# Kernel optimization log

Hardware: AMD Instinct MI355X
Metric: run time of the kernel (lower is better)

## Reference

```python
import math
import jax, jax.numpy as jnp
from jax import lax
import numpy as np

NUM_HEADS = 8

def conv2d(x, w, b):
    # x: [N,C,H,W], w: [O,I,3,3], padding=1 == SAME
    y = lax.conv_general_dilated(x, w, (1, 1), 'SAME',
                                 dimension_numbers=('NCHW', 'OIHW', 'NCHW'))
    return y + b[None, :, None, None]

def setup_inputs() -> dict:
    key = jax.random.key(0)
    ks = jax.random.split(key, 10)
    B, L, C = 64, 196, 768
    K, R = 8192, 8
    return {
        'in_feas': jax.random.normal(ks[0], (B, L, C), jnp.float32),
        'cur_f': 4,
        'codebook': jax.random.normal(ks[1], (K, C), jnp.float32),
        'att_w': jax.random.normal(ks[2], (R, C, 3, 3), jnp.float32) * 0.02,
        'att_b': jnp.zeros((R,), jnp.float32),
        'ex_w': jax.random.normal(ks[3], (1, C, 3, 3), jnp.float32) * 0.02,
        'ex_b': jnp.zeros((1,), jnp.float32),
        'qkv_w': jax.random.normal(ks[4], (3 * C, C), jnp.float32) * 0.02,
        'qkv_b': jnp.zeros((3 * C,), jnp.float32),
        'proj_w': jax.random.normal(ks[5], (C, C), jnp.float32) * 0.02,
        'proj_b': jnp.zeros((C,), jnp.float32),
    }

def attention(x, qkv_w, qkv_b, proj_w, proj_b):
    # x: [B, N, C], standard multi-head self-attention
    B, N, C = x.shape
    dh = C // NUM_HEADS
    qkv = x @ qkv_w.T + qkv_b                          # [B,N,3C]
    qkv = qkv.reshape(B, N, 3, NUM_HEADS, dh).transpose(2, 0, 3, 1, 4)
    q, k, v = qkv[0], qkv[1], qkv[2]                   # [B,H,N,dh]
    attn = jax.nn.softmax(jnp.einsum('bhnd,bhmd->bhnm', q, k) * (dh ** -0.5), axis=-1)
    out = jnp.einsum('bhnm,bhmd->bhnd', attn, v)
    out = out.transpose(0, 2, 1, 3).reshape(B, N, C)
    return out @ proj_w.T + proj_b

def reference(in_feas, cur_f, codebook, att_w, att_b, ex_w, ex_b,
              qkv_w, qkv_b, proj_w, proj_b):
    B, L, C = in_feas.shape
    h = int(math.sqrt(L)); w = L // h
    R = att_w.shape[0]

    # ---- Vector quantization: cdist + argmin + codebook gather ----
    flat = in_feas.reshape(-1, C)                      # [B*L, C]
    d = (jnp.sum(flat * flat, axis=1, keepdims=True)
         - 2.0 * flat @ codebook.T
         + jnp.sum(codebook * codebook, axis=1)[None, :])   # [B*L, K]
    idx = jnp.argmin(d, axis=1)                        # [B*L]
    quant = codebook[idx]                              # gather
    vq = flat + lax.stop_gradient(quant - flat)        # straight-through
    enc = idx.reshape(-1, h, w)                        # [B, h, w]

    # ---- Motion excitation (cur_f > 1) ----
    Bp = B // cur_f
    x = in_feas.reshape(Bp, cur_f, L, C)
    diff = x - jnp.concatenate([x[:, :1], x[:, :-1]], axis=1)  # frame diff, first frame zero
    dmap = diff.reshape(-1, L, C).transpose(0, 2, 1).reshape(-1, C, h, w)
    mm = conv2d(dmap, ex_w, ex_b).reshape(Bp, cur_f, L)
    mm = jax.nn.softmax(mm, axis=-1)
    motion = (x * mm[..., None]).reshape(-1, C)
    vq = vq + motion

    # ---- Aggregation: region attention conv + masked pooling (as one einsum) ----
    xm = vq.reshape(B, L, C).transpose(0, 2, 1).reshape(B, C, h, w)
    region_mask = conv2d(xm, att_w, att_b)             # [B,R,h,w]
    regions = jnp.einsum('bchw,brhw->bcr', xm, region_mask) / (h * w)  # [B,C,R]
    vd = regions.transpose(0, 2, 1)                    # [B,R,C]

    # ---- Interaction: self-attention over T*S region tokens ----
    seq = vd.reshape(Bp, cur_f * R, C)
    seq = attention(seq, qkv_w, qkv_b, proj_w, proj_b)
    vd = seq.reshape(-1, R, C)                         # [B,R,C]
    return (vd, enc, region_mask)
```

## Files before the change

kernel.cpp:

```cpp
#include <hip/hip_runtime.h>
#include <math.h>

#define B_   64
#define L_   196
#define C_   768
#define K_   8192
#define R_   8
#define HW_  14
#define M_   (B_*L_)
#define NH_  8
#define DH_  96
#define BP_  16
#define NT_  32

typedef unsigned short ushort_t;
typedef __attribute__((ext_vector_type(8))) short short8v;
typedef __attribute__((ext_vector_type(4))) float f32x4;
typedef __attribute__((ext_vector_type(4))) int   i32x4;

#define BIGF __uint_as_float(0x7F000000u)

__device__ inline float wave_reduce_sum(float v) {
    #pragma unroll
    for (int o = 32; o >= 1; o >>= 1) v += __shfl_xor(v, o, 64);
    return v;
}
__device__ inline float wave_reduce_max(float v) {
    #pragma unroll
    for (int o = 32; o >= 1; o >>= 1) v = fmaxf(v, __shfl_xor(v, o, 64));
    return v;
}

__device__ inline ushort_t f2bf_rne(float f) {
    unsigned u = __float_as_uint(f);
    unsigned r = u + 0x7fffu + ((u >> 16) & 1u);
    return (ushort_t)(r >> 16);
}
__device__ inline float bf2f(ushort_t h) { return __uint_as_float(((unsigned)h) << 16); }

__device__ inline char q8(float f, float s) {
    int q = __float2int_rn(f * s);
    return (char)(q < -127 ? -127 : (q > 127 ? 127 : q));
}

__device__ inline void gload_lds16(const void* gsrc, void* ldst) {
    __builtin_amdgcn_global_load_lds(
        (const __attribute__((address_space(1))) unsigned int*)gsrc,
        (__attribute__((address_space(3))) unsigned int*)ldst, 16, 0, 0);
}

__global__ __launch_bounds__(256) void cbq_kernel(const float* __restrict__ CB,
                                                  char* __restrict__ CBq,
                                                  float* __restrict__ cnq) {
    __shared__ float xs[16 * 776];
    const int t = threadIdx.x;
    const int blk = blockIdx.x;
    const float4* src = (const float4*)(CB + (size_t)blk * 16 * C_);
    #pragma unroll
    for (int i = 0; i < 12; ++i) {
        int idx4 = t + i * 256;
        int r = idx4 / 192, c4 = idx4 - r * 192;
        ((float4*)(xs + r * 776))[c4] = src[idx4];
    }
    __syncthreads();
    #pragma unroll
    for (int i = 0; i < 3; ++i) {
        int s = t + i * 256;
        int kb = s >> 6, l = s & 63;
        int row = l & 15;
        int k0 = kb * 64 + ((l >> 4) << 4);
        union { char c[16]; i32x4 v; } Q;
        #pragma unroll
        for (int e = 0; e < 16; ++e) Q.c[e] = q8(xs[row * 776 + k0 + e], 32.f);
        *(i32x4*)&CBq[(((size_t)blk * 12 + kb) << 10) + l * 16] = Q.v;
    }
    int row = t & 15, chunk = t >> 4;
    float sum = 0.f;
    #pragma unroll
    for (int j = 0; j < 48; ++j) { float v = xs[row * 776 + chunk * 48 + j]; sum += v * v; }
    sum += __shfl_xor(sum, 16, 64);
    sum += __shfl_xor(sum, 32, 64);
    __shared__ float red[4][16];
    if ((t & 63) < 16) red[t >> 6][t & 15] = sum;
    __syncthreads();
    if (t < 16) cnq[blk * 16 + t] = (red[0][t] + red[1][t] + red[2][t] + red[3][t]) * 1024.f;
}

__global__ __launch_bounds__(256) void aq_kernel(const float* __restrict__ X,
                                                 char* __restrict__ Aq) {
    __shared__ float xs[16 * 776];
    const int t = threadIdx.x;
    const int rg = blockIdx.x;
    const float4* src = (const float4*)(X + (size_t)rg * 16 * C_);
    #pragma unroll
    for (int i = 0; i < 12; ++i) {
        int idx4 = t + i * 256;
        int r = idx4 / 192, c4 = idx4 - r * 192;
        ((float4*)(xs + r * 776))[c4] = src[idx4];
    }
    __syncthreads();
    #pragma unroll
    for (int i = 0; i < 3; ++i) {
        int s = t + i * 256;
        int kb = s >> 6, l = s & 63;
        int row = l & 15;
        int k0 = kb * 64 + ((l >> 4) << 4);
        union { char c[16]; i32x4 v; } Q;
        #pragma unroll
        for (int e = 0; e < 16; ++e) Q.c[e] = q8(xs[row * 776 + k0 + e], 32.f);
        *(i32x4*)&Aq[(((size_t)rg * 12 + kb) << 10) + l * 16] = Q.v;
    }
}

__global__ __launch_bounds__(256) void wsplit_kernel(const float* __restrict__ att_w,
                                                     const float* __restrict__ ex_w,
                                                     ushort_t* __restrict__ attHi,
                                                     char* __restrict__ exq) {
    int gid = blockIdx.x * 256 + threadIdx.x;
    if (gid < 7680) {
        int cb = gid / 1536;
        int rem = gid - cb * 1536;
        int l = rem & 63;
        int col = cb * 16 + (l & 15);
        int k = ((rem >> 6) << 5) + ((l >> 4) << 3);
        union { ushort_t u[8]; short8v v; } H;
        #pragma unroll
        for (int e = 0; e < 8; ++e) {
            int c = k + e;
            float f = (col < 72) ? att_w[(size_t)(col & 7) * 6912 + c * 9 + (col >> 3)] : 0.f;
            H.u[e] = f2bf_rne(f);
        }
        *(short8v*)&attHi[(size_t)gid * 8] = H.v;
    } else if (gid < 8448) {
        int g2 = gid - 7680;
        int l = g2 & 63;
        int col = l & 15;
        int k0 = ((g2 >> 6) << 6) + ((l >> 4) << 4);
        union { char c[16]; i32x4 v; } Q;
        #pragma unroll
        for (int e = 0; e < 16; ++e) {
            int k = k0 + e;
            float f = (col < 9) ? ex_w[k * 9 + col] : 0.f;
            Q.c[e] = q8(f, 1024.f);
        }
        *(i32x4*)&exq[(size_t)g2 * 16] = Q.v;
    }
}

__global__ __launch_bounds__(256) void wgemm_split_kernel(const float* __restrict__ qkv_w,
                                                          const float* __restrict__ proj_w,
                                                          ushort_t* __restrict__ wqkvF,
                                                          ushort_t* __restrict__ wprojF) {
    int gid = blockIdx.x * 256 + threadIdx.x;
    const float* W; ushort_t* D; int g2;
    if (gid < 221184) { W = qkv_w; D = wqkvF; g2 = gid; }
    else { W = proj_w; D = wprojF; g2 = gid - 221184; }
    int cb = g2 / 1536;
    int rem = g2 - cb * 1536;
    int l = rem & 63;
    int col = cb * 16 + (l & 15);
    int k = ((rem >> 6) << 5) + ((l >> 4) << 3);
    union { ushort_t u[8]; short8v v; } H;
    #pragma unroll
    for (int e = 0; e < 8; ++e) H.u[e] = f2bf_rne(W[(size_t)col * 768 + k + e]);
    *(short8v*)&D[(size_t)g2 * 8] = H.v;
}

__global__ __launch_bounds__(256, 2) void vq_i8_kernel(const char* __restrict__ Aq,
                                                       const char* __restrict__ CBq,
                                                       const float* __restrict__ cnq,
                                                       float2* __restrict__ cand) {
    __shared__ __align__(16) char AqL[2][4096];
    __shared__ __align__(16) char BqL[2][32768];
    const int tid = threadIdx.x;
    const int l = tid & 63, w = tid >> 6;
    const int g = blockIdx.x;
    const int mt = blockIdx.y;
    const int row0 = mt * 64;
    const int rg0 = mt * 4;

    int K[9];
    #pragma unroll
    for (int i = 0; i < 9; ++i) {
        int s = w * 9 + i;
        K[i] = ((s < 4) ? (rg0 + s) * 12288 : (g * 64 + (s - 4)) * 12288) + l * 16;
    }
    float cnr[2][8];
    #pragma unroll
    for (int ch = 0; ch < 2; ++ch)
        #pragma unroll
        for (int nf = 0; nf < 8; ++nf)
            cnr[ch][nf] = cnq[g * 1024 + ch * 512 + w * 128 + nf * 16 + (l & 15)];

    float v1[4][4], v2[4][4];
    #pragma unroll
    for (int mf = 0; mf < 4; ++mf)
        #pragma unroll
        for (int rg = 0; rg < 4; ++rg) { v1[mf][rg] = BIGF; v2[mf][rg] = BIGF; }

    auto STAGE = [&](int buf, int oA, int oB) {
        #pragma unroll
        for (int i = 0; i < 9; ++i) {
            int s = w * 9 + i;
            if (s < 4)
                gload_lds16((const char*)Aq + (unsigned)(K[i] + oA), &AqL[buf][s << 10]);
            else
                gload_lds16((const char*)CBq + (unsigned)(K[i] + oB), &BqL[buf][(s - 4) << 10]);
        }
    };

    int cur = 0;
    STAGE(0, 0, 0);
    __syncthreads();
    int sA = 1024, sB = 1024;

    #pragma unroll 1
    for (int ch = 0; ch < 2; ++ch) {
        i32x4 acc[4][8];
        #pragma unroll
        for (int mf = 0; mf < 4; ++mf)
            #pragma unroll
            for (int nf = 0; nf < 8; ++nf) acc[mf][nf] = (i32x4){0, 0, 0, 0};

        #pragma unroll 1
        for (int st = 0; st < 12; ++st) {
            int u = ch * 12 + st;
            if (u < 23) {
                STAGE(cur ^ 1, sA, sB);
                bool wrap = (((u + 1) % 12) == 11);
                sA += wrap ? -11264 : 1024;
                sB += wrap ? 381952 : 1024;
            }
            const char* aB = &AqL[cur][l * 16];
            const char* bB = &BqL[cur][(w * 8) * 1024 + l * 16];
            i32x4 aq[4];
            #pragma unroll
            for (int mf = 0; mf < 4; ++mf)
                aq[mf] = *(const i32x4*)(aB + (mf << 10));
            __builtin_amdgcn_s_setprio(1);
            #pragma unroll
            for (int nf = 0; nf < 8; ++nf) {
                i32x4 bq = *(const i32x4*)(bB + (nf << 10));
                #pragma unroll
                for (int mf = 0; mf < 4; ++mf)
                    acc[mf][nf] = __builtin_amdgcn_mfma_i32_16x16x64_i8(aq[mf], bq, acc[mf][nf], 0, 0, 0);
            }
            __builtin_amdgcn_s_setprio(0);
            asm volatile("s_waitcnt vmcnt(9)" ::: "memory");
            __builtin_amdgcn_sched_barrier(0);
            __builtin_amdgcn_s_barrier();
            __builtin_amdgcn_sched_barrier(0);
            cur ^= 1;
        }
        #pragma unroll
        for (int nf = 0; nf < 8; ++nf) {
            float cnv = cnr[ch][nf];
            unsigned tag = ((unsigned)ch << 7) | ((unsigned)nf << 4) | (unsigned)(l & 15);
            #pragma unroll
            for (int mf = 0; mf < 4; ++mf)
                #pragma unroll
                for (int rg = 0; rg < 4; ++rg) {
                    float d = fmaf(-2.f, (float)acc[mf][nf][rg], cnv);
                    float dp = __uint_as_float((__float_as_uint(d) & 0xFFFFFF00u) | tag);
                    float t = fmaxf(v1[mf][rg], dp);
                    v1[mf][rg] = fminf(v1[mf][rg], dp);
                    v2[mf][rg] = fminf(v2[mf][rg], t);
                }
        }
    }
    #pragma unroll
    for (int mf = 0; mf < 4; ++mf)
        #pragma unroll
        for (int rg = 0; rg < 4; ++rg) {
            float a1 = v1[mf][rg], a2 = v2[mf][rg];
            #pragma unroll
            for (int off = 8; off >= 1; off >>= 1) {
                float b1 = __shfl_xor(a1, off, 64), b2 = __shfl_xor(a2, off, 64);
                float m1 = fminf(a1, b1);
                float t  = fmaxf(a1, b1);
                a2 = fminf(t, fminf(a2, b2));
                a1 = m1;
            }
            if ((l & 15) == 0) {
                int row = row0 + mf * 16 + (l >> 4) * 4 + rg;
                cand[(size_t)row * 32 + g * 4 + w] = make_float2(a1, a2);
            }
        }
}

__global__ __launch_bounds__(256) void rescore_kernel(const float2* __restrict__ cand,
                                                      const float* __restrict__ X,
                                                      const float* __restrict__ CB,
                                                      int* __restrict__ idx,
                                                      float* __restrict__ encOut) {
    int w = threadIdx.x >> 6, l = threadIdx.x & 63;
    int r = blockIdx.x * 4 + w;
    float a0, a1, a2, a3;
    if (l < 32) {
        float2 c = cand[(size_t)r * 32 + l];
        unsigned b0 = __float_as_uint(c.x), b1 = __float_as_uint(c.y);
        a0 = __uint_as_float((b0 & 0xFFFFE000u) | ((unsigned)l << 8) | (b0 & 0xFFu));
        a1 = __uint_as_float((b1 & 0xFFFFE000u) | ((unsigned)l << 8) | (b1 & 0xFFu));
    } else { a0 = BIGF; a1 = BIGF; }
    a2 = BIGF; a3 = BIGF;
    #pragma unroll
    for (int off = 32; off >= 1; off >>= 1) {
        float b0 = __shfl_xor(a0, off, 64), b1 = __shfl_xor(a1, off, 64);
        float b2 = __shfl_xor(a2, off, 64), b3 = __shfl_xor(a3, off, 64);
        a0 = fminf(a0, b3); a1 = fminf(a1, b2);
        a2 = fminf(a2, b1); a3 = fminf(a3, b0);
        float lo, hi;
        lo = fminf(a0, a2); hi = fmaxf(a0, a2); a0 = lo; a2 = hi;
        lo = fminf(a1, a3); hi = fmaxf(a1, a3); a1 = lo; a3 = hi;
        lo = fminf(a0, a1); hi = fmaxf(a0, a1); a0 = lo; a1 = hi;
        lo = fminf(a2, a3); hi = fmaxf(a2, a3); a2 = lo; a3 = hi;
    }
    int jc[4];
    float av[4] = {a0, a1, a2, a3};
    #pragma unroll
    for (int k = 0; k < 4; ++k) {
        unsigned bits = __float_as_uint(av[k]);
        int s = (bits >> 8) & 31;
        jc[k] = (s >> 2) * 1024 + (int)((bits >> 7) & 1) * 512 + (s & 3) * 128
              + (int)((bits >> 4) & 7) * 16 + (int)(bits & 15);
    }
    int j0 = jc[0], j1 = jc[1], j2 = jc[2], j3 = jc[3];
    double dot0 = 0, dot1 = 0, dot2 = 0, dot3 = 0;
    double nn0 = 0, nn1 = 0, nn2 = 0, nn3 = 0;
    const float* xr = X + (size_t)r * C_;
    #pragma unroll
    for (int jj = 0; jj < 12; ++jj) {
        int c = l * 12 + jj;
        double x = (double)xr[c];
        double c0 = (double)CB[(size_t)j0 * C_ + c]; dot0 += x * c0; nn0 += c0 * c0;
        double c1 = (double)CB[(size_t)j1 * C_ + c]; dot1 += x * c1; nn1 += c1 * c1;
        double c2 = (double)CB[(size_t)j2 * C_ + c]; dot2 += x * c2; nn2 += c2 * c2;
        double c3 = (double)CB[(size_t)j3 * C_ + c]; dot3 += x * c3; nn3 += c3 * c3;
    }
    #pragma unroll
    for (int off = 32; off >= 1; off >>= 1) {
        dot0 += __shfl_xor(dot0, off, 64); dot1 += __shfl_xor(dot1, off, 64);
        dot2 += __shfl_xor(dot2, off, 64); dot3 += __shfl_xor(dot3, off, 64);
        nn0 += __shfl_xor(nn0, off, 64); nn1 += __shfl_xor(nn1, off, 64);
        nn2 += __shfl_xor(nn2, off, 64); nn3 += __shfl_xor(nn3, off, 64);
    }
    if (l == 0) {
        double d0 = nn0 - 2.0 * dot0, d1 = nn1 - 2.0 * dot1;
        double d2 = nn2 - 2.0 * dot2, d3 = nn3 - 2.0 * dot3;
        double best = d0; int bi = j0;
        if (d1 < best || (d1 == best && j1 < bi)) { best = d1; bi = j1; }
        if (d2 < best || (d2 == best && j2 < bi)) { best = d2; bi = j2; }
        if (d3 < best || (d3 == best && j3 < bi)) { best = d3; bi = j3; }
        idx[r] = bi;
        encOut[r] = (float)bi;
    }
}

__global__ __launch_bounds__(256) void convgemm_i8_kernel(const char* __restrict__ Aq,
                                                          const char* __restrict__ Bq,
                                                          float* __restrict__ out) {
    __shared__ __align__(16) char AqL[8 * 1024];
    __shared__ __align__(16) char BqL[1024];
    const int tid = threadIdx.x;
    const int l = tid & 63, w = tid >> 6;
    const int rg0 = blockIdx.x * 8, row0 = blockIdx.x * 128;
    i32x4 acc[2];
    acc[0] = (i32x4){0, 0, 0, 0}; acc[1] = (i32x4){0, 0, 0, 0};
    #pragma unroll 1
    for (int st = 0; st < 12; ++st) {
        __syncthreads();
        #pragma unroll
        for (int i = 0; i < 3; ++i) {
            int s = w * 3 + i;
            if (s < 8)
                gload_lds16(&Aq[(((size_t)(rg0 + s) * 12 + st) << 10) + l * 16], &AqL[s << 10]);
            else if (s == 8)
                gload_lds16(&Bq[((size_t)st << 10) + l * 16], &BqL[0]);
        }
        __syncthreads();
        i32x4 bq = *(const i32x4*)&BqL[l * 16];
        #pragma unroll
        for (int mf = 0; mf < 2; ++mf) {
            i32x4 aq = *(const i32x4*)&AqL[((w * 2 + mf) << 10) + l * 16];
            acc[mf] = __builtin_amdgcn_mfma_i32_16x16x64_i8(aq, bq, acc[mf], 0, 0, 0);
        }
    }
    #pragma unroll
    for (int mf = 0; mf < 2; ++mf)
        #pragma unroll
        for (int rg = 0; rg < 4; ++rg) {
            int row = row0 + w * 32 + mf * 16 + (l >> 4) * 4 + rg;
            out[(size_t)row * 16 + (l & 15)] = (float)acc[mf][rg] * (1.f / 32768.f);
        }
}

template<int NF>
__global__ __launch_bounds__(256) void convgemm_kernel(const ushort_t* __restrict__ Ahi_g,
                                                       const ushort_t* __restrict__ Bhi_g,
                                                       float* __restrict__ out) {
    __shared__ __align__(16) ushort_t AhL[16 * 512];
    __shared__ __align__(16) ushort_t BhL[NF * 2 * 512];
    const int TOT = 16 + 2 * NF;
    const int PW = (TOT + 3) >> 2;
    const int tid = threadIdx.x;
    const int l = tid & 63, w = tid >> 6;
    const int rg0 = blockIdx.x * 8;
    const int row0 = blockIdx.x * 128;
    f32x4 acc[2][NF];
    #pragma unroll
    for (int mf = 0; mf < 2; ++mf)
        #pragma unroll
        for (int nf = 0; nf < NF; ++nf) acc[mf][nf] = (f32x4){0.f, 0.f, 0.f, 0.f};
    #pragma unroll 1
    for (int st = 0; st < 12; ++st) {
        __syncthreads();
        #pragma unroll
        for (int i = 0; i < PW; ++i) {
            int s = w * PW + i;
            if (s < 16) {
                int rb = s >> 1, kb = s & 1;
                gload_lds16(&Ahi_g[(((size_t)(rg0 + rb) * 24 + st * 2 + kb) << 9) + l * 8], &AhL[s << 9]);
            } else if (s < TOT) {
                int t2 = s - 16;
                int cb = t2 >> 1, kb = t2 & 1;
                gload_lds16(&Bhi_g[(((size_t)cb * 24 + st * 2 + kb) << 9) + l * 8], &BhL[t2 << 9]);
            }
        }
        __syncthreads();
        #pragma unroll
        for (int kf = 0; kf < 2; ++kf) {
            short8v ah[2];
            #pragma unroll
            for (int mf = 0; mf < 2; ++mf)
                ah[mf] = *(const short8v*)&AhL[(((w * 2 + mf) * 2 + kf) << 9) + l * 8];
            #pragma unroll
            for (int nf = 0; nf < NF; ++nf) {
                short8v bh = *(const short8v*)&BhL[((nf * 2 + kf) << 9) + l * 8];
                #pragma unroll
                for (int mf = 0; mf < 2; ++mf)
                    acc[mf][nf] = __builtin_amdgcn_mfma_f32_16x16x32_bf16(ah[mf], bh, acc[mf][nf], 0, 0, 0);
            }
        }
    }
    #pragma unroll
    for (int mf = 0; mf < 2; ++mf)
        #pragma unroll
        for (int nf = 0; nf < NF; ++nf)
            #pragma unroll
            for (int rg = 0; rg < 4; ++rg) {
                int row = row0 + w * 32 + mf * 16 + (l >> 4) * 4 + rg;
                out[(size_t)row * (NF * 16) + nf * 16 + (l & 15)] = acc[mf][nf][rg];
            }
}

template<int NF>
__global__ __launch_bounds__(256) void gemm_frag_kernel(const ushort_t* __restrict__ Af,
                                                        const ushort_t* __restrict__ Bf,
                                                        const float* __restrict__ bias,
                                                        float* __restrict__ out, int N) {
    __shared__ __align__(16) ushort_t AhL[16 * 512];
    __shared__ __align__(16) ushort_t BhL[2 * NF * 512];
    const int TOT = 16 + 2 * NF;
    const int PW = (TOT + 3) >> 2;
    const int tid = threadIdx.x;
    const int l = tid & 63, w = tid >> 6;
    const int rg0 = blockIdx.x * 8, row0 = blockIdx.x * 128;
    const int cb0 = blockIdx.y * NF;
    f32x4 acc[2][NF];
    #pragma unroll
    for (int mf = 0; mf < 2; ++mf)
        #pragma unroll
        for (int nf = 0; nf < NF; ++nf) acc[mf][nf] = (f32x4){0.f, 0.f, 0.f, 0.f};
    #pragma unroll 1
    for (int st = 0; st < 12; ++st) {
        __syncthreads();
        #pragma unroll
        for (int i = 0; i < PW; ++i) {
            int s = w * PW + i;
            if (s < 16) {
                int rb = s >> 1, kb = s & 1;
                gload_lds16(&Af[(((size_t)(rg0 + rb) * 24 + st * 2 + kb) << 9) + l * 8], &AhL[s << 9]);
            } else if (s < TOT) {
                int t2 = s - 16;
                int cb = t2 >> 1, kb = t2 & 1;
                gload_lds16(&Bf[(((size_t)(cb0 + cb) * 24 + st * 2 + kb) << 9) + l * 8], &BhL[t2 << 9]);
            }
        }
        __syncthreads();
        #pragma unroll
        for (int kf = 0; kf < 2; ++kf) {
            short8v ah[2];
            #pragma unroll
            for (int mf = 0; mf < 2; ++mf)
                ah[mf] = *(const short8v*)&AhL[(((w * 2 + mf) * 2 + kf) << 9) + l * 8];
            #pragma unroll
            for (int nf = 0; nf < NF; ++nf) {
                short8v bh = *(const short8v*)&BhL[((nf * 2 + kf) << 9) + l * 8];
                #pragma unroll
                for (int mf = 0; mf < 2; ++mf)
                    acc[mf][nf] = __builtin_amdgcn_mfma_f32_16x16x32_bf16(ah[mf], bh, acc[mf][nf], 0, 0, 0);
            }
        }
    }
    #pragma unroll
    for (int mf = 0; mf < 2; ++mf)
        #pragma unroll
        for (int nf = 0; nf < NF; ++nf) {
            int col = (cb0 + nf) * 16 + (l & 15);
            float bv = bias[col];
            #pragma unroll
            for (int rg = 0; rg < 4; ++rg) {
                int row = row0 + w * 32 + mf * 16 + (l >> 4) * 4 + rg;
                out[(size_t)row * N + col] = acc[mf][nf][rg] + bv;
            }
        }
}

__global__ __launch_bounds__(256) void mm_finish_kernel(const float* __restrict__ XW,
                                                        const float* __restrict__ ex_b,
                                                        float* __restrict__ sm) {
    int b = blockIdx.x, t = threadIdx.x;
    float val = -INFINITY;
    if (t < L_) {
        if ((b & 3) == 0) val = ex_b[0];
        else {
            int yy = t / HW_, xx = t - (t / HW_) * HW_;
            float acc = 0.f;
            #pragma unroll
            for (int dy = 0; dy < 3; ++dy) {
                int sy = yy + dy - 1; if (sy < 0 || sy >= HW_) continue;
                #pragma unroll
                for (int dx = 0; dx < 3; ++dx) {
                    int sx = xx + dx - 1; if (sx < 0 || sx >= HW_) continue;
                    int q = sy * HW_ + sx, tap = dy * 3 + dx;
                    acc += XW[((size_t)b * L_ + q) * 16 + tap]
                         - XW[((size_t)(b - 1) * L_ + q) * 16 + tap];
                }
            }
            val = acc + ex_b[0];
        }
    }
    __shared__ float red[4];
    float mw = wave_reduce_max(val);
    if ((t & 63) == 0) red[t >> 6] = mw;
    __syncthreads();
    float mx = fmaxf(fmaxf(red[0], red[1]), fmaxf(red[2], red[3]));
    float e = (t < L_) ? expf(val - mx) : 0.f;
    __syncthreads();
    float sw = wave_reduce_sum(e);
    if ((t & 63) == 0) red[t >> 6] = sw;
    __syncthreads();
    float s = red[0] + red[1] + red[2] + red[3];
    if (t < L_) sm[b * L_ + t] = e / s;
}

__global__ __launch_bounds__(256) void vqf_split_kernel(const float* __restrict__ X,
                                                        const float* __restrict__ CB,
                                                        const int* __restrict__ idx,
                                                        const float* __restrict__ sm,
                                                        ushort_t* __restrict__ Vhi) {
    const int rg = blockIdx.x, t = threadIdx.x;
    #pragma unroll
    for (int i = 0; i < 6; ++i) {
        int s = t + i * 256;
        int kb = s >> 6, l = s & 63;
        int row = rg * 16 + (l & 15);
        int k = kb * 32 + ((l >> 4) << 3);
        int kidx = idx[row];
        float sc = sm[row];
        const float* xp = &X[(size_t)row * C_ + k];
        const float* cp = &CB[(size_t)kidx * C_ + k];
        union { ushort_t u[8]; short8v v; } H;
        #pragma unroll
        for (int e = 0; e < 8; ++e) H.u[e] = f2bf_rne(cp[e] + xp[e] * sc);
        *(short8v*)&Vhi[((size_t)rg * 1536 + s) * 8] = H.v;
    }
}

__global__ __launch_bounds__(256) void rm_finish_kernel(const float* __restrict__ OUTC,
                                                        const float* __restrict__ att_b,
                                                        float* __restrict__ rmOut) {
    int gid = blockIdx.x * 256 + threadIdx.x;
    if (gid >= B_ * R_ * L_) return;
    int b = gid / (R_ * L_);
    int rem = gid - b * (R_ * L_);
    int r = rem / L_, p = rem - r * L_;
    int yy = p / HW_, xx = p - yy * HW_;
    float acc = att_b[r];
    #pragma unroll
    for (int dy = 0; dy < 3; ++dy) {
        int sy = yy + dy - 1; if (sy < 0 || sy >= HW_) continue;
        #pragma unroll
        for (int dx = 0; dx < 3; ++dx) {
            int sx = xx + dx - 1; if (sx < 0 || sx >= HW_) continue;
            int q = sy * HW_ + sx, tap = dy * 3 + dx;
            acc += OUTC[((size_t)b * L_ + q) * 80 + tap * 8 + r];
        }
    }
    rmOut[gid] = acc;
}

__global__ __launch_bounds__(256) void regions_kernel(const ushort_t* __restrict__ Vhi,
                                                      const float* __restrict__ rm,
                                                      ushort_t* __restrict__ seqF) {
    int b = blockIdx.x, cg = blockIdx.y, t = threadIdx.x;
    __shared__ float rms[R_ * L_];
    for (int i = t; i < R_ * L_; i += 256) rms[i] = rm[(size_t)b * R_ * L_ + i];
    __syncthreads();
    const float inv = 1.f / 196.f;
    int c = cg * 256 + t;
    int kb = c >> 5, q = (c >> 3) & 3, e = c & 7;
    float acc[R_] = {};
    for (int p = 0; p < L_; ++p) {
        int row = b * L_ + p;
        int rg = row >> 4, rr = row & 15;
        size_t a = (((size_t)rg * 24 + kb) * 64 + q * 16 + rr) * 8 + e;
        float x = bf2f(Vhi[a]);
        #pragma unroll
        for (int r = 0; r < R_; ++r) acc[r] += x * rms[r * L_ + p];
    }
    #pragma unroll
    for (int r = 0; r < R_; ++r) {
        int row = b * 8 + r;
        int rg2 = row >> 4, rr = row & 15;
        seqF[(((size_t)rg2 * 24 + kb) * 64 + q * 16 + rr) * 8 + e] = f2bf_rne(acc[r] * inv);
    }
}

__global__ __launch_bounds__(256) void attn_kernel(const float* __restrict__ qkv,
                                                   ushort_t* __restrict__ outF) {
    int bp = blockIdx.x, h = blockIdx.y;
    __shared__ float qs[NT_][DH_], ks[NT_][DH_], vs[NT_][DH_];
    __shared__ float sc[NT_][NT_ + 1];
    int tid = threadIdx.x;
    for (int e = tid; e < NT_ * DH_; e += 256) {
        int n = e / DH_, d = e - n * DH_;
        size_t base = ((size_t)(bp * NT_ + n)) * 2304 + h * DH_ + d;
        qs[n][d] = qkv[base];
        ks[n][d] = qkv[base + 768];
        vs[n][d] = qkv[base + 1536];
    }
    __syncthreads();
    const float scale = 1.0f / sqrtf((float)DH_);
    for (int e = tid; e < NT_ * NT_; e += 256) {
        int n = e >> 5, m = e & 31;
        float s = 0.f;
        #pragma unroll 8
        for (int d = 0; d < DH_; ++d) s += qs[n][d] * ks[m][d];
        sc[n][m] = s * scale;
    }
    __syncthreads();
    if (tid < NT_) {
        float mx = -INFINITY;
        #pragma unroll
        for (int m = 0; m < NT_; ++m) mx = fmaxf(mx, sc[tid][m]);
        float sum = 0.f;
        #pragma unroll
        for (int m = 0; m < NT_; ++m) { float e2 = expf(sc[tid][m] - mx); sc[tid][m] = e2; sum += e2; }
        float inv = 1.f / sum;
        #pragma unroll
        for (int m = 0; m < NT_; ++m) sc[tid][m] *= inv;
    }
    __syncthreads();
    for (int e = tid; e < NT_ * DH_; e += 256) {
        int n = e / DH_, d = e - n * DH_;
        float o = 0.f;
        #pragma unroll
        for (int m = 0; m < NT_; ++m) o += sc[n][m] * vs[m][d];
        int row = bp * NT_ + n, c = h * DH_ + d;
        outF[(((size_t)(row >> 4) * 24 + (c >> 5)) * 64 + ((c >> 3) & 3) * 16 + (row & 15)) * 8 + (c & 7)]
            = f2bf_rne(o);
    }
}

extern "C" void kernel_launch(void* const* d_in, const int* in_sizes, int n_in,
                              void* d_out, int out_size, void* d_ws, size_t ws_size,
                              hipStream_t stream) {
    const float* in_feas  = (const float*)d_in[0];
    const float* codebook = (const float*)d_in[2];
    const float* att_w    = (const float*)d_in[3];
    const float* att_b    = (const float*)d_in[4];
    const float* ex_w     = (const float*)d_in[5];
    const float* ex_b     = (const float*)d_in[6];
    const float* qkv_w    = (const float*)d_in[7];
    const float* qkv_b    = (const float*)d_in[8];
    const float* proj_w   = (const float*)d_in[9];
    const float* proj_b   = (const float*)d_in[10];

    float* out    = (float*)d_out;
    float* outVd  = out;
    float* outEnc = out + 393216;
    float* outRm  = out + 393216 + 12544;

    float* ws = (float*)d_ws;
    float*    cnq    = ws + 0;
    float2*   cand   = (float2*)(ws + 8192);
    char*     CBq    = (char*)(ws + 1613824);
    char*     Aq     = (char*)(ws + 3186688);
    ushort_t* attHi  = (ushort_t*)(ws + 5595136);
    char*     exq    = (char*)(ws + 5625856);
    ushort_t* wqkvF  = (ushort_t*)(ws + 5628928);
    ushort_t* wprojF = (ushort_t*)(ws + 6513664);
    int*      idx    = (int*)(ws + 6808576);
    float*    XW     = ws + 6821120;
    float*    sm     = ws + 7021824;
    ushort_t* Vhi    = (ushort_t*)(ws + 7034368);
    float*    OUTC   = ws + 11851264;
    ushort_t* seqF   = (ushort_t*)(ws + 12854784);
    float*    qkvb   = ws + 13051392;
    ushort_t* attnbF = (ushort_t*)(ws + 14231040);

    hipLaunchKernelGGL(cbq_kernel, dim3(512), dim3(256), 0, stream, codebook, CBq, cnq);
    hipLaunchKernelGGL(aq_kernel, dim3(784), dim3(256), 0, stream, in_feas, Aq);
    hipLaunchKernelGGL(wsplit_kernel, dim3(33), dim3(256), 0, stream, att_w, ex_w, attHi, exq);
    hipLaunchKernelGGL(wgemm_split_kernel, dim3(1152), dim3(256), 0, stream,
                       qkv_w, proj_w, wqkvF, wprojF);
    hipLaunchKernelGGL(vq_i8_kernel, dim3(8, 196), dim3(256), 0, stream, Aq, CBq, cnq, cand);
    hipLaunchKernelGGL(convgemm_i8_kernel, dim3(98), dim3(256), 0, stream, Aq, exq, XW);
    hipLaunchKernelGGL(rescore_kernel, dim3(M_ / 4), dim3(256), 0, stream,
                       cand, in_feas, codebook, idx, outEnc);
    hipLaunchKernelGGL(mm_finish_kernel, dim3(B_), dim3(256), 0, stream, XW, ex_b, sm);
    hipLaunchKernelGGL(vqf_split_kernel, dim3(784), dim3(256), 0, stream,
                       in_feas, codebook, idx, sm, Vhi);
    hipLaunchKernelGGL((convgemm_kernel<5>), dim3(98), dim3(256), 0, stream, Vhi, attHi, OUTC);
    hipLaunchKernelGGL(rm_finish_kernel, dim3(392), dim3(256), 0, stream, OUTC, att_b, outRm);
    hipLaunchKernelGGL(regions_kernel, dim3(B_, 3), dim3(256), 0, stream, Vhi, outRm, seqF);
    hipLaunchKernelGGL((gemm_frag_kernel<8>), dim3(4, 18), dim3(256), 0, stream,
                       seqF, wqkvF, qkv_b, qkvb, 2304);
    hipLaunchKernelGGL(attn_kernel, dim3(BP_, NH_), dim3(256), 0, stream, qkvb, attnbF);
    hipLaunchKernelGGL((gemm_frag_kernel<8>), dim3(4, 6), dim3(256), 0, stream,
                       attnbF, wprojF, proj_b, outVd, 768);
}
```

Baseline: 312.6 us.

## Merge prep kernels, narrow VQ tiles for occupancy, fuse rescore/convgemm and rm_finish

Four preprocessing kernels (codebook/activation int8 quantisation, weight splits) become one prep_kernel. The int8 VQ GEMM now covers half as many codebook columns per block across twice as many blocks, with smaller LDS buffers, launch bounds of 3 blocks per CU and a reworked wait/barrier placement. The rescore kernel carries explicit indices through the top-4 shuffle merge and shares a launch with the int8 excitation conv GEMM. The region-mask finish is folded into regions_kernel, which costs recomputation across the three channel groups. Fewer launches and higher VQ occupancy are the goal, at the price of more candidates per row (64 instead of 32) and more rescoring shuffle work.

```diff
diff --git a/kernel.cpp b/kernel.cpp
--- a/kernel.cpp
+++ b/kernel.cpp
@@ -49,129 +49,121 @@
         (__attribute__((address_space(3))) unsigned int*)ldst, 16, 0, 0);
 }
 
-__global__ __launch_bounds__(256) void cbq_kernel(const float* __restrict__ CB,
-                                                  char* __restrict__ CBq,
-                                                  float* __restrict__ cnq) {
+__device__ inline void ce4(float& v0, int& j0, float& v1, int& j1) {
+    bool sw = (v1 < v0) || (v1 == v0 && j1 < j0);
+    float tv = sw ? v1 : v0, uv = sw ? v0 : v1;
+    int tj = sw ? j1 : j0, uj = sw ? j0 : j1;
+    v0 = tv; j0 = tj; v1 = uv; j1 = uj;
+}
+__device__ inline void pickmin(float& v, int& j, float bv, int bj) {
+    if (bv < v || (bv == v && bj < j)) { v = bv; j = bj; }
+}
+
+__global__ __launch_bounds__(256) void prep_kernel(const float* __restrict__ CB,
+                                                   const float* __restrict__ X,
+                                                   const float* __restrict__ att_w,
+                                                   const float* __restrict__ ex_w,
+                                                   const float* __restrict__ qkv_w,
+                                                   const float* __restrict__ proj_w,
+                                                   char* __restrict__ CBq,
+                                                   float* __restrict__ cnq,
+                                                   char* __restrict__ Aq,
+                                                   ushort_t* __restrict__ attHi,
+                                                   char* __restrict__ exq,
+                                                   ushort_t* __restrict__ wqkvF,
+                                                   ushort_t* __restrict__ wprojF) {
     __shared__ float xs[16 * 776];
+    __shared__ float red[4][16];
+    const int bid = blockIdx.x;
     const int t = threadIdx.x;
-    const int blk = blockIdx.x;
-    const float4* src = (const float4*)(CB + (size_t)blk * 16 * C_);
-    #pragma unroll
-    for (int i = 0; i < 12; ++i) {
-        int idx4 = t + i * 256;
-        int r = idx4 / 192, c4 = idx4 - r * 192;
-        ((float4*)(xs + r * 776))[c4] = src[idx4];
-    }
-    __syncthreads();
-    #pragma unroll
-    for (int i = 0; i < 3; ++i) {
-        int s = t + i * 256;
-        int kb = s >> 6, l = s & 63;
-        int row = l & 15;
-        int k0 = kb * 64 + ((l >> 4) << 4);
-        union { char c[16]; i32x4 v; } Q;
-        #pragma unroll
-        for (int e = 0; e < 16; ++e) Q.c[e] = q8(xs[row * 776 + k0 + e], 32.f);
-        *(i32x4*)&CBq[(((size_t)blk * 12 + kb) << 10) + l * 16] = Q.v;
-    }
-    int row = t & 15, chunk = t >> 4;
-    float sum = 0.f;
-    #pragma unroll
-    for (int j = 0; j < 48; ++j) { float v = xs[row * 776 + chunk * 48 + j]; sum += v * v; }
-    sum += __shfl_xor(sum, 16, 64);
-    sum += __shfl_xor(sum, 32, 64);
-    __shared__ float red[4][16];
-    if ((t & 63) < 16) red[t >> 6][t & 15] = sum;
-    __syncthreads();
-    if (t < 16) cnq[blk * 16 + t] = (red[0][t] + red[1][t] + red[2][t] + red[3][t]) * 1024.f;
-}
-
-__global__ __launch_bounds__(256) void aq_kernel(const float* __restrict__ X,
-                                                 char* __restrict__ Aq) {
-    __shared__ float xs[16 * 776];
-    const int t = threadIdx.x;
-    const int rg = blockIdx.x;
-    const float4* src = (const float4*)(X + (size_t)rg * 16 * C_);
-    #pragma unroll
-    for (int i = 0; i < 12; ++i) {
-        int idx4 = t + i * 256;
-        int r = idx4 / 192, c4 = idx4 - r * 192;
-        ((float4*)(xs + r * 776))[c4] = src[idx4];
-    }
-    __syncthreads();
-    #pragma unroll
-    for (int i = 0; i < 3; ++i) {
-        int s = t + i * 256;
-        int kb = s >> 6, l = s & 63;
-        int row = l & 15;
-        int k0 = kb * 64 + ((l >> 4) << 4);
-        union { char c[16]; i32x4 v; } Q;
-        #pragma unroll
-        for (int e = 0; e < 16; ++e) Q.c[e] = q8(xs[row * 776 + k0 + e], 32.f);
-        *(i32x4*)&Aq[(((size_t)rg * 12 + kb) << 10) + l * 16] = Q.v;
-    }
-}
-
-__global__ __launch_bounds__(256) void wsplit_kernel(const float* __restrict__ att_w,
-                                                     const float* __restrict__ ex_w,
-                                                     ushort_t* __restrict__ attHi,
-                                                     char* __restrict__ exq) {
-    int gid = blockIdx.x * 256 + threadIdx.x;
-    if (gid < 7680) {
-        int cb = gid / 1536;
-        int rem = gid - cb * 1536;
+    if (bid < 1296) {
+        const bool isCB = bid < 512;
+        const int blk = isCB ? bid : bid - 512;
+        const float* src0 = isCB ? CB : X;
+        char* dst = isCB ? CBq : Aq;
+        const float4* src = (const float4*)(src0 + (size_t)blk * 16 * C_);
+        #pragma unroll
+        for (int i = 0; i < 12; ++i) {
+            int idx4 = t + i * 256;
+            int r = idx4 / 192, c4 = idx4 - r * 192;
+            ((float4*)(xs + r * 776))[c4] = src[idx4];
+        }
+        __syncthreads();
+        #pragma unroll
+        for (int i = 0; i < 3; ++i) {
+            int s = t + i * 256;
+            int kb = s >> 6, l = s & 63;
+            int row = l & 15;
+            int k0 = kb * 64 + ((l >> 4) << 4);
+            union { char c[16]; i32x4 v; } Q;
+            #pragma unroll
+            for (int e = 0; e < 16; ++e) Q.c[e] = q8(xs[row * 776 + k0 + e], 32.f);
+            *(i32x4*)&dst[(((size_t)blk * 12 + kb) << 10) + l * 16] = Q.v;
+        }
+        if (isCB) {
+            int row = t & 15, chunk = t >> 4;
+            float sum = 0.f;
+            #pragma unroll
+            for (int j = 0; j < 48; ++j) { float v = xs[row * 776 + chunk * 48 + j]; sum += v * v; }
+            sum += __shfl_xor(sum, 16, 64);
+            sum += __shfl_xor(sum, 32, 64);
+            if ((t & 63) < 16) red[t >> 6][t & 15] = sum;
+            __syncthreads();
+            if (t < 16) cnq[blk * 16 + t] = (red[0][t] + red[1][t] + red[2][t] + red[3][t]) * 1024.f;
+        }
+    } else if (bid < 1329) {
+        int gid = (bid - 1296) * 256 + t;
+        if (gid < 7680) {
+            int cb = gid / 1536;
+            int rem = gid - cb * 1536;
+            int l = rem & 63;
+            int col = cb * 16 + (l & 15);
+            int k = ((rem >> 6) << 5) + ((l >> 4) << 3);
+            union { ushort_t u[8]; short8v v; } H;
+            #pragma unroll
+            for (int e = 0; e < 8; ++e) {
+                int c = k + e;
+                float f = (col < 72) ? att_w[(size_t)(col & 7) * 6912 + c * 9 + (col >> 3)] : 0.f;
+                H.u[e] = f2bf_rne(f);
+            }
+            *(short8v*)&attHi[(size_t)gid * 8] = H.v;
+        } else if (gid < 8448) {
+            int g2 = gid - 7680;
+            int l = g2 & 63;
+            int col = l & 15;
+            int k0 = ((g2 >> 6) << 6) + ((l >> 4) << 4);
+            union { char c[16]; i32x4 v; } Q;
+            #pragma unroll
+            for (int e = 0; e < 16; ++e) {
+                int k = k0 + e;
+                float f = (col < 9) ? ex_w[k * 9 + col] : 0.f;
+                Q.c[e] = q8(f, 1024.f);
+            }
+            *(i32x4*)&exq[(size_t)g2 * 16] = Q.v;
+        }
+    } else {
+        int gid = (bid - 1329) * 256 + t;
+        const float* W; ushort_t* D; int g2;
+        if (gid < 221184) { W = qkv_w; D = wqkvF; g2 = gid; }
+        else { W = proj_w; D = wprojF; g2 = gid - 221184; }
+        int cb = g2 / 1536;
+        int rem = g2 - cb * 1536;
         int l = rem & 63;
         int col = cb * 16 + (l & 15);
         int k = ((rem >> 6) << 5) + ((l >> 4) << 3);
         union { ushort_t u[8]; short8v v; } H;
         #pragma unroll
-        for (int e = 0; e < 8; ++e) {
-            int c = k + e;
-            float f = (col < 72) ? att_w[(size_t)(col & 7) * 6912 + c * 9 + (col >> 3)] : 0.f;
-            H.u[e] = f2bf_rne(f);
-        }
-        *(short8v*)&attHi[(size_t)gid * 8] = H.v;
-    } else if (gid < 8448) {
-        int g2 = gid - 7680;
-        int l = g2 & 63;
-        int col = l & 15;
-        int k0 = ((g2 >> 6) << 6) + ((l >> 4) << 4);
-        union { char c[16]; i32x4 v; } Q;
-        #pragma unroll
-        for (int e = 0; e < 16; ++e) {
-            int k = k0 + e;
-            float f = (col < 9) ? ex_w[k * 9 + col] : 0.f;
-            Q.c[e] = q8(f, 1024.f);
-        }
-        *(i32x4*)&exq[(size_t)g2 * 16] = Q.v;
-    }
-}
-
-__global__ __launch_bounds__(256) void wgemm_split_kernel(const float* __restrict__ qkv_w,
-                                                          const float* __restrict__ proj_w,
-                                                          ushort_t* __restrict__ wqkvF,
-                                                          ushort_t* __restrict__ wprojF) {
-    int gid = blockIdx.x * 256 + threadIdx.x;
-    const float* W; ushort_t* D; int g2;
-    if (gid < 221184) { W = qkv_w; D = wqkvF; g2 = gid; }
-    else { W = proj_w; D = wprojF; g2 = gid - 221184; }
-    int cb = g2 / 1536;
-    int rem = g2 - cb * 1536;
-    int l = rem & 63;
-    int col = cb * 16 + (l & 15);
-    int k = ((rem >> 6) << 5) + ((l >> 4) << 3);
-    union { ushort_t u[8]; short8v v; } H;
-    #pragma unroll
-    for (int e = 0; e < 8; ++e) H.u[e] = f2bf_rne(W[(size_t)col * 768 + k + e]);
-    *(short8v*)&D[(size_t)g2 * 8] = H.v;
-}
-
-__global__ __launch_bounds__(256, 2) void vq_i8_kernel(const char* __restrict__ Aq,
+        for (int e = 0; e < 8; ++e) H.u[e] = f2bf_rne(W[(size_t)col * 768 + k + e]);
+        *(short8v*)&D[(size_t)g2 * 8] = H.v;
+    }
+}
+
+__global__ __launch_bounds__(256, 3) void vq_i8_kernel(const char* __restrict__ Aq,
                                                        const char* __restrict__ CBq,
                                                        const float* __restrict__ cnq,
                                                        float2* __restrict__ cand) {
     __shared__ __align__(16) char AqL[2][4096];
-    __shared__ __align__(16) char BqL[2][32768];
+    __shared__ __align__(16) char BqL[2][16384];
     const int tid = threadIdx.x;
     const int l = tid & 63, w = tid >> 6;
     const int g = blockIdx.x;
@@ -179,18 +171,18 @@
     const int row0 = mt * 64;
     const int rg0 = mt * 4;
 
-    int K[9];
-    #pragma unroll
-    for (int i = 0; i < 9; ++i) {
-        int s = w * 9 + i;
-        K[i] = ((s < 4) ? (rg0 + s) * 12288 : (g * 64 + (s - 4)) * 12288) + l * 16;
-    }
-    float cnr[2][8];
+    int K[5];
+    #pragma unroll
+    for (int i = 0; i < 5; ++i) {
+        int s = w * 5 + i;
+        K[i] = ((s < 4) ? (rg0 + s) * 12288 : (g * 32 + (s - 4)) * 12288) + l * 16;
+    }
+    float cnr[2][4];
     #pragma unroll
     for (int ch = 0; ch < 2; ++ch)
         #pragma unroll
-        for (int nf = 0; nf < 8; ++nf)
-            cnr[ch][nf] = cnq[g * 1024 + ch * 512 + w * 128 + nf * 16 + (l & 15)];
+        for (int nf = 0; nf < 4; ++nf)
+            cnr[ch][nf] = cnq[g * 512 + ch * 256 + (w * 4 + nf) * 16 + (l & 15)];
 
     float v1[4][4], v2[4][4];
     #pragma unroll
@@ -200,8 +192,8 @@
 
     auto STAGE = [&](int buf, int oA, int oB) {
         #pragma unroll
-        for (int i = 0; i < 9; ++i) {
-            int s = w * 9 + i;
+        for (int i = 0; i < 5; ++i) {
+            int s = w * 5 + i;
             if (s < 4)
                 gload_lds16((const char*)Aq + (unsigned)(K[i] + oA), &AqL[buf][s << 10]);
             else
@@ -211,16 +203,15 @@
 
     int cur = 0;
     STAGE(0, 0, 0);
-    __syncthreads();
     int sA = 1024, sB = 1024;
 
     #pragma unroll 1
     for (int ch = 0; ch < 2; ++ch) {
-        i32x4 acc[4][8];
+        i32x4 acc[4][4];
         #pragma unroll
         for (int mf = 0; mf < 4; ++mf)
             #pragma unroll
-            for (int nf = 0; nf < 8; ++nf) acc[mf][nf] = (i32x4){0, 0, 0, 0};
+            for (int nf = 0; nf < 4; ++nf) acc[mf][nf] = (i32x4){0, 0, 0, 0};
 
         #pragma unroll 1
         for (int st = 0; st < 12; ++st) {
@@ -229,33 +220,36 @@
                 STAGE(cur ^ 1, sA, sB);
                 bool wrap = (((u + 1) % 12) == 11);
                 sA += wrap ? -11264 : 1024;
-                sB += wrap ? 381952 : 1024;
-            }
-            const char* aB = &AqL[cur][l * 16];
-            const char* bB = &BqL[cur][(w * 8) * 1024 + l * 16];
+                sB += wrap ? 185344 : 1024;
+                asm volatile("s_waitcnt vmcnt(5)" ::: "memory");
+            } else {
+                asm volatile("s_waitcnt vmcnt(0)" ::: "memory");
+            }
+            __builtin_amdgcn_sched_barrier(0);
+            __builtin_amdgcn_s_barrier();
+            __builtin_amdgcn_sched_barrier(0);
             i32x4 aq[4];
             #pragma unroll
             for (int mf = 0; mf < 4; ++mf)
-                aq[mf] = *(const i32x4*)(aB + (mf << 10));
+                aq[mf] = *(const i32x4*)&AqL[cur][(mf << 10) + l * 16];
             __builtin_amdgcn_s_setprio(1);
             #pragma unroll
-            for (int nf = 0; nf < 8; ++nf) {
-                i32x4 bq = *(const i32x4*)(bB + (nf << 10));
+            for (int nf = 0; nf < 4; ++nf) {
+                i32x4 bq = *(const i32x4*)&BqL[cur][((w * 4 + nf) << 10) + l * 16];
                 #pragma unroll
                 for (int mf = 0; mf < 4; ++mf)
                     acc[mf][nf] = __builtin_amdgcn_mfma_i32_16x16x64_i8(aq[mf], bq, acc[mf][nf], 0, 0, 0);
             }
             __builtin_amdgcn_s_setprio(0);
-            asm volatile("s_waitcnt vmcnt(9)" ::: "memory");
             __builtin_amdgcn_sched_barrier(0);
             __builtin_amdgcn_s_barrier();
             __builtin_amdgcn_sched_barrier(0);
             cur ^= 1;
         }
         #pragma unroll
-        for (int nf = 0; nf < 8; ++nf) {
+        for (int nf = 0; nf < 4; ++nf) {
             float cnv = cnr[ch][nf];
-            unsigned tag = ((unsigned)ch << 7) | ((unsigned)nf << 4) | (unsigned)(l & 15);
+            unsigned tag = ((unsigned)ch << 6) | ((unsigned)nf << 4) | (unsigned)(l & 15);
             #pragma unroll
             for (int mf = 0; mf < 4; ++mf)
                 #pragma unroll
@@ -283,115 +277,105 @@
             }
             if ((l & 15) == 0) {
                 int row = row0 + mf * 16 + (l >> 4) * 4 + rg;
-                cand[(size_t)row * 32 + g * 4 + w] = make_float2(a1, a2);
-            }
-        }
-}
-
-__global__ __launch_bounds__(256) void rescore_kernel(const float2* __restrict__ cand,
-                                                      const float* __restrict__ X,
-                                                      const float* __restrict__ CB,
-                                                      int* __restrict__ idx,
-                                                      float* __restrict__ encOut) {
-    int w = threadIdx.x >> 6, l = threadIdx.x & 63;
-    int r = blockIdx.x * 4 + w;
-    float a0, a1, a2, a3;
-    if (l < 32) {
-        float2 c = cand[(size_t)r * 32 + l];
-        unsigned b0 = __float_as_uint(c.x), b1 = __float_as_uint(c.y);
-        a0 = __uint_as_float((b0 & 0xFFFFE000u) | ((unsigned)l << 8) | (b0 & 0xFFu));
-        a1 = __uint_as_float((b1 & 0xFFFFE000u) | ((unsigned)l << 8) | (b1 & 0xFFu));
-    } else { a0 = BIGF; a1 = BIGF; }
-    a2 = BIGF; a3 = BIGF;
-    #pragma unroll
-    for (int off = 32; off >= 1; off >>= 1) {
-        float b0 = __shfl_xor(a0, off, 64), b1 = __shfl_xor(a1, off, 64);
-        float b2 = __shfl_xor(a2, off, 64), b3 = __shfl_xor(a3, off, 64);
-        a0 = fminf(a0, b3); a1 = fminf(a1, b2);
-        a2 = fminf(a2, b1); a3 = fminf(a3, b0);
-        float lo, hi;
-        lo = fminf(a0, a2); hi = fmaxf(a0, a2); a0 = lo; a2 = hi;
-        lo = fminf(a1, a3); hi = fmaxf(a1, a3); a1 = lo; a3 = hi;
-        lo = fminf(a0, a1); hi = fmaxf(a0, a1); a0 = lo; a1 = hi;
-        lo = fminf(a2, a3); hi = fmaxf(a2, a3); a2 = lo; a3 = hi;
-    }
-    int jc[4];
-    float av[4] = {a0, a1, a2, a3};
-    #pragma unroll
-    for (int k = 0; k < 4; ++k) {
-        unsigned bits = __float_as_uint(av[k]);
-        int s = (bits >> 8) & 31;
-        jc[k] = (s >> 2) * 1024 + (int)((bits >> 7) & 1) * 512 + (s & 3) * 128
-              + (int)((bits >> 4) & 7) * 16 + (int)(bits & 15);
-    }
-    int j0 = jc[0], j1 = jc[1], j2 = jc[2], j3 = jc[3];
-    double dot0 = 0, dot1 = 0, dot2 = 0, dot3 = 0;
-    double nn0 = 0, nn1 = 0, nn2 = 0, nn3 = 0;
-    const float* xr = X + (size_t)r * C_;
-    #pragma unroll
-    for (int jj = 0; jj < 12; ++jj) {
-        int c = l * 12 + jj;
-        double x = (double)xr[c];
-        double c0 = (double)CB[(size_t)j0 * C_ + c]; dot0 += x * c0; nn0 += c0 * c0;
-        double c1 = (double)CB[(size_t)j1 * C_ + c]; dot1 += x * c1; nn1 += c1 * c1;
-        double c2 = (double)CB[(size_t)j2 * C_ + c]; dot2 += x * c2; nn2 += c2 * c2;
-        double c3 = (double)CB[(size_t)j3 * C_ + c]; dot3 += x * c3; nn3 += c3 * c3;
-    }
-    #pragma unroll
-    for (int off = 32; off >= 1; off >>= 1) {
-        dot0 += __shfl_xor(dot0, off, 64); dot1 += __shfl_xor(dot1, off, 64);
-        dot2 += __shfl_xor(dot2, off, 64); dot3 += __shfl_xor(dot3, off, 64);
-        nn0 += __shfl_xor(nn0, off, 64); nn1 += __shfl_xor(nn1, off, 64);
-        nn2 += __shfl_xor(nn2, off, 64); nn3 += __shfl_xor(nn3, off, 64);
-    }
-    if (l == 0) {
-        double d0 = nn0 - 2.0 * dot0, d1 = nn1 - 2.0 * dot1;
-        double d2 = nn2 - 2.0 * dot2, d3 = nn3 - 2.0 * dot3;
-        double best = d0; int bi = j0;
-        if (d1 < best || (d1 == best && j1 < bi)) { best = d1; bi = j1; }
-        if (d2 < best || (d2 == best && j2 < bi)) { best = d2; bi = j2; }
-        if (d3 < best || (d3 == best && j3 < bi)) { best = d3; bi = j3; }
-        idx[r] = bi;
-        encOut[r] = (float)bi;
-    }
-}
-
-__global__ __launch_bounds__(256) void convgemm_i8_kernel(const char* __restrict__ Aq,
-                                                          const char* __restrict__ Bq,
-                                                          float* __restrict__ out) {
+                cand[(size_t)row * 64 + g * 4 + w] = make_float2(a1, a2);
+            }
+        }
+}
+
+__global__ __launch_bounds__(256) void post1_kernel(const char* __restrict__ Aq,
+                                                    const char* __restrict__ exq,
+                                                    float* __restrict__ XW,
+                                                    const float2* __restrict__ cand,
+                                                    const float* __restrict__ X,
+                                                    const float* __restrict__ CB,
+                                                    int* __restrict__ idx,
+                                                    float* __restrict__ encOut) {
     __shared__ __align__(16) char AqL[8 * 1024];
     __shared__ __align__(16) char BqL[1024];
-    const int tid = threadIdx.x;
-    const int l = tid & 63, w = tid >> 6;
-    const int rg0 = blockIdx.x * 8, row0 = blockIdx.x * 128;
-    i32x4 acc[2];
-    acc[0] = (i32x4){0, 0, 0, 0}; acc[1] = (i32x4){0, 0, 0, 0};
-    #pragma unroll 1
-    for (int st = 0; st < 12; ++st) {
-        __syncthreads();
-        #pragma unroll
-        for (int i = 0; i < 3; ++i) {
-            int s = w * 3 + i;
-            if (s < 8)
-                gload_lds16(&Aq[(((size_t)(rg0 + s) * 12 + st) << 10) + l * 16], &AqL[s << 10]);
-            else if (s == 8)
-                gload_lds16(&Bq[((size_t)st << 10) + l * 16], &BqL[0]);
-        }
-        __syncthreads();
-        i32x4 bq = *(const i32x4*)&BqL[l * 16];
-        #pragma unroll
-        for (int mf = 0; mf < 2; ++mf) {
-            i32x4 aq = *(const i32x4*)&AqL[((w * 2 + mf) << 10) + l * 16];
-            acc[mf] = __builtin_amdgcn_mfma_i32_16x16x64_i8(aq, bq, acc[mf], 0, 0, 0);
-        }
-    }
-    #pragma unroll
-    for (int mf = 0; mf < 2; ++mf)
-        #pragma unroll
-        for (int rg = 0; rg < 4; ++rg) {
-            int row = row0 + w * 32 + mf * 16 + (l >> 4) * 4 + rg;
-            out[(size_t)row * 16 + (l & 15)] = (float)acc[mf][rg] * (1.f / 32768.f);
-        }
+    if (blockIdx.x < 98) {
+        const int tid = threadIdx.x;
+        const int l = tid & 63, w = tid >> 6;
+        const int rg0 = blockIdx.x * 8, row0 = blockIdx.x * 128;
+        i32x4 acc[2];
+        acc[0] = (i32x4){0, 0, 0, 0}; acc[1] = (i32x4){0, 0, 0, 0};
+        #pragma unroll 1
+        for (int st = 0; st < 12; ++st) {
+            __syncthreads();
+            #pragma unroll
+            for (int i = 0; i < 3; ++i) {
+                int s = w * 3 + i;
+                if (s < 8)
+                    gload_lds16(&Aq[(((size_t)(rg0 + s) * 12 + st) << 10) + l * 16], &AqL[s << 10]);
+                else if (s == 8)
+                    gload_lds16(&exq[((size_t)st << 10) + l * 16], &BqL[0]);
+            }
+            __syncthreads();
+            i32x4 bq = *(const i32x4*)&BqL[l * 16];
+            #pragma unroll
+            for (int mf = 0; mf < 2; ++mf) {
+                i32x4 aq = *(const i32x4*)&AqL[((w * 2 + mf) << 10) + l * 16];
+                acc[mf] = __builtin_amdgcn_mfma_i32_16x16x64_i8(aq, bq, acc[mf], 0, 0, 0);
+            }
+        }
+        #pragma unroll
+        for (int mf = 0; mf < 2; ++mf)
+            #pragma unroll
+            for (int rg = 0; rg < 4; ++rg) {
+                int row = row0 + w * 32 + mf * 16 + (l >> 4) * 4 + rg;
+                XW[(size_t)row * 16 + (l & 15)] = (float)acc[mf][rg] * (1.f / 32768.f);
+            }
+    } else {
+        int bid = blockIdx.x - 98;
+        int w4 = threadIdx.x >> 6, l = threadIdx.x & 63;
+        int r = bid * 4 + w4;
+        float2 c = cand[(size_t)r * 64 + l];
+        unsigned b0 = __float_as_uint(c.x), b1 = __float_as_uint(c.y);
+        int gg = l >> 2, ww = l & 3;
+        int j0 = gg * 512 + (int)((b0 >> 6) & 1) * 256 + (ww * 4 + (int)((b0 >> 4) & 3)) * 16 + (int)(b0 & 15);
+        int j1 = gg * 512 + (int)((b1 >> 6) & 1) * 256 + (ww * 4 + (int)((b1 >> 4) & 3)) * 16 + (int)(b1 & 15);
+        float a0 = c.x, a1 = c.y, a2 = BIGF, a3 = BIGF;
+        int j2 = 0x7fffffff, j3 = 0x7fffffff;
+        #pragma unroll
+        for (int off = 32; off >= 1; off >>= 1) {
+            float b0f = __shfl_xor(a0, off, 64), b1f = __shfl_xor(a1, off, 64);
+            float b2f = __shfl_xor(a2, off, 64), b3f = __shfl_xor(a3, off, 64);
+            int p0 = __shfl_xor(j0, off, 64), p1 = __shfl_xor(j1, off, 64);
+            int p2 = __shfl_xor(j2, off, 64), p3 = __shfl_xor(j3, off, 64);
+            pickmin(a0, j0, b3f, p3); pickmin(a1, j1, b2f, p2);
+            pickmin(a2, j2, b1f, p1); pickmin(a3, j3, b0f, p0);
+            ce4(a0, j0, a2, j2); ce4(a1, j1, a3, j3);
+            ce4(a0, j0, a1, j1); ce4(a2, j2, a3, j3);
+        }
+        double dot0 = 0, dot1 = 0, dot2 = 0, dot3 = 0;
+        double nn0 = 0, nn1 = 0, nn2 = 0, nn3 = 0;
+        const float* xr = X + (size_t)r * C_;
+        #pragma unroll
+        for (int jj = 0; jj < 12; ++jj) {
+            int cc = l * 12 + jj;
+            double x = (double)xr[cc];
+            double c0 = (double)CB[(size_t)j0 * C_ + cc]; dot0 += x * c0; nn0 += c0 * c0;
+            double c1 = (double)CB[(size_t)j1 * C_ + cc]; dot1 += x * c1; nn1 += c1 * c1;
+            double c2 = (double)CB[(size_t)j2 * C_ + cc]; dot2 += x * c2; nn2 += c2 * c2;
+            double c3 = (double)CB[(size_t)j3 * C_ + cc]; dot3 += x * c3; nn3 += c3 * c3;
+        }
+        #pragma unroll
+        for (int off = 32; off >= 1; off >>= 1) {
+            dot0 += __shfl_xor(dot0, off, 64); dot1 += __shfl_xor(dot1, off, 64);
+            dot2 += __shfl_xor(dot2, off, 64); dot3 += __shfl_xor(dot3, off, 64);
+            nn0 += __shfl_xor(nn0, off, 64); nn1 += __shfl_xor(nn1, off, 64);
+            nn2 += __shfl_xor(nn2, off, 64); nn3 += __shfl_xor(nn3, off, 64);
+        }
+        if (l == 0) {
+            double d0 = nn0 - 2.0 * dot0, d1 = nn1 - 2.0 * dot1;
+            double d2 = nn2 - 2.0 * dot2, d3 = nn3 - 2.0 * dot3;
+            double best = d0; int bi = j0;
+            if (d1 < best || (d1 == best && j1 < bi)) { best = d1; bi = j1; }
+            if (d2 < best || (d2 == best && j2 < bi)) { best = d2; bi = j2; }
+            if (d3 < best || (d3 == best && j3 < bi)) { best = d3; bi = j3; }
+            idx[r] = bi;
+            encOut[r] = (float)bi;
+        }
+    }
 }
 
 template<int NF>
@@ -577,35 +561,30 @@
     }
 }
 
-__global__ __launch_bounds__(256) void rm_finish_kernel(const float* __restrict__ OUTC,
-                                                        const float* __restrict__ att_b,
-                                                        float* __restrict__ rmOut) {
-    int gid = blockIdx.x * 256 + threadIdx.x;
-    if (gid >= B_ * R_ * L_) return;
-    int b = gid / (R_ * L_);
-    int rem = gid - b * (R_ * L_);
-    int r = rem / L_, p = rem - r * L_;
-    int yy = p / HW_, xx = p - yy * HW_;
-    float acc = att_b[r];
-    #pragma unroll
-    for (int dy = 0; dy < 3; ++dy) {
-        int sy = yy + dy - 1; if (sy < 0 || sy >= HW_) continue;
-        #pragma unroll
-        for (int dx = 0; dx < 3; ++dx) {
-            int sx = xx + dx - 1; if (sx < 0 || sx >= HW_) continue;
-            int q = sy * HW_ + sx, tap = dy * 3 + dx;
-            acc += OUTC[((size_t)b * L_ + q) * 80 + tap * 8 + r];
-        }
-    }
-    rmOut[gid] = acc;
-}
-
 __global__ __launch_bounds__(256) void regions_kernel(const ushort_t* __restrict__ Vhi,
-                                                      const float* __restrict__ rm,
+                                                      const float* __restrict__ OUTC,
+                                                      const float* __restrict__ att_b,
+                                                      float* __restrict__ rmOut,
                                                       ushort_t* __restrict__ seqF) {
     int b = blockIdx.x, cg = blockIdx.y, t = threadIdx.x;
     __shared__ float rms[R_ * L_];
-    for (int i = t; i < R_ * L_; i += 256) rms[i] = rm[(size_t)b * R_ * L_ + i];
+    for (int i = t; i < R_ * L_; i += 256) {
+        int r = i / L_, p = i - r * L_;
+        int yy = p / HW_, xx = p - yy * HW_;
+        float acc = att_b[r];
+        #pragma unroll
+        for (int dy = 0; dy < 3; ++dy) {
+            int sy = yy + dy - 1; if (sy < 0 || sy >= HW_) continue;
+            #pragma unroll
+            for (int dx = 0; dx < 3; ++dx) {
+                int sx = xx + dx - 1; if (sx < 0 || sx >= HW_) continue;
+                int q = sy * HW_ + sx, tap = dy * 3 + dx;
+                acc += OUTC[((size_t)b * L_ + q) * 80 + tap * 8 + r];
+            }
+        }
+        rms[i] = acc;
+        if (cg == 0) rmOut[((size_t)b * R_ + r) * L_ + p] = acc;
+    }
     __syncthreads();
     const float inv = 1.f / 196.f;
     int c = cg * 256 + t;
@@ -710,21 +689,18 @@
     float*    qkvb   = ws + 13051392;
     ushort_t* attnbF = (ushort_t*)(ws + 14231040);
 
-    hipLaunchKernelGGL(cbq_kernel, dim3(512), dim3(256), 0, stream, codebook, CBq, cnq);
-    hipLaunchKernelGGL(aq_kernel, dim3(784), dim3(256), 0, stream, in_feas, Aq);
-    hipLaunchKernelGGL(wsplit_kernel, dim3(33), dim3(256), 0, stream, att_w, ex_w, attHi, exq);
-    hipLaunchKernelGGL(wgemm_split_kernel, dim3(1152), dim3(256), 0, stream,
-                       qkv_w, proj_w, wqkvF, wprojF);
-    hipLaunchKernelGGL(vq_i8_kernel, dim3(8, 196), dim3(256), 0, stream, Aq, CBq, cnq, cand);
-    hipLaunchKernelGGL(convgemm_i8_kernel, dim3(98), dim3(256), 0, stream, Aq, exq, XW);
-    hipLaunchKernelGGL(rescore_kernel, dim3(M_ / 4), dim3(256), 0, stream,
-                       cand, in_feas, codebook, idx, outEnc);
+    hipLaunchKernelGGL(prep_kernel, dim3(2481), dim3(256), 0, stream,
+                       codebook, in_feas, att_w, ex_w, qkv_w, proj_w,
+                       CBq, cnq, Aq, attHi, exq, wqkvF, wprojF);
+    hipLaunchKernelGGL(vq_i8_kernel, dim3(16, 196), dim3(256), 0, stream, Aq, CBq, cnq, cand);
+    hipLaunchKernelGGL(post1_kernel, dim3(98 + 3136), dim3(256), 0, stream,
+                       Aq, exq, XW, cand, in_feas, codebook, idx, outEnc);
     hipLaunchKernelGGL(mm_finish_kernel, dim3(B_), dim3(256), 0, stream, XW, ex_b, sm);
     hipLaunchKernelGGL(vqf_split_kernel, dim3(784), dim3(256), 0, stream,
                        in_feas, codebook, idx, sm, Vhi);
     hipLaunchKernelGGL((convgemm_kernel<5>), dim3(98), dim3(256), 0, stream, Vhi, attHi, OUTC);
-    hipLaunchKernelGGL(rm_finish_kernel, dim3(392), dim3(256), 0, stream, OUTC, att_b, outRm);
-    hipLaunchKernelGGL(regions_kernel, dim3(B_, 3), dim3(256), 0, stream, Vhi, outRm, seqF);
+    hipLaunchKernelGGL(regions_kernel, dim3(B_, 3), dim3(256), 0, stream,
+                       Vhi, OUTC, att_b, outRm, seqF);
     hipLaunchKernelGGL((gemm_frag_kernel<8>), dim3(4, 18), dim3(256), 0, stream,
                        seqF, wqkvF, qkv_b, qkvb, 2304);
     hipLaunchKernelGGL(attn_kernel, dim3(BP_, NH_), dim3(256), 0, stream, qkvb, attnbF);
```

New measurement: 298.9 us. -4.4%, faster.
